# Performance work log

Measured on AMD Instinct MI355X. Metric: run time of the kernel, lower is better.

The kernel has to match this reference:

```python
import jax, jax.numpy as jnp
import numpy as np

# Production-scale config
N_NODES = 2048      # nodes in input graph
N_UND_EDGES = 4096  # undirected edges (avg degree ~4)
LABELS = 16         # node label categories
FILTERS = 16        # number of learned filter graphs
FNODES = 8          # nodes per filter graph ('nodes' init arg)
HOPS = 3            # egonet radius
MAX_EGO = 128       # egonet padding (covers typical 3-hop size at deg~4)
WL_LEVELS = 4       # initial labels + 3 WL refinements (n_iter=3)


def _mix(h):
    # 32-bit integer hash (lowbias32); equal colors -> equal hash, distinct w.h.p.
    h = h ^ (h >> jnp.uint32(16))
    h = h * jnp.uint32(0x7FEB352D)
    h = h ^ (h >> jnp.uint32(15))
    h = h * jnp.uint32(0x846CA68B)
    h = h ^ (h >> jnp.uint32(16))
    return h


def _wl_step(adj_u32, h):
    # multiset-hash WL relabel: new color = hash(old color, sum of hashed neighbor colors)
    msg = jnp.einsum('guv,gv->gu', adj_u32, _mix(h))  # uint32 wraparound sum
    return _mix(h * jnp.uint32(0x9E3779B1) + msg)


def _max_cc_mask(B):
    # largest connected component of a small binary graph via min-label propagation
    M = B.shape[0]
    lbl = jnp.arange(M)
    Bb = B > 0
    for _ in range(M):
        nb = jnp.min(jnp.where(Bb, lbl[None, :], M), axis=1)
        lbl = jnp.minimum(lbl, nb)
    cnt = (lbl[:, None] == lbl[None, :]).sum(1)
    return lbl == lbl[jnp.argmax(cnt)]


def setup_inputs() -> dict:
    key = jax.random.key(0)
    k1, k2, k3, k4, k5 = jax.random.split(key, 5)
    x = jax.random.normal(k1, (N_NODES, LABELS), dtype=jnp.float32)
    src = jax.random.randint(k2, (N_UND_EDGES,), 0, N_NODES)
    dst = jax.random.randint(k3, (N_UND_EDGES,), 0, N_NODES)
    edge_index = jnp.stack([jnp.concatenate([src, dst]),
                            jnp.concatenate([dst, src])]).astype(jnp.int32)
    batch = jnp.zeros((N_NODES,), dtype=jnp.int32)
    # filter adjacency exactly as in GKernel.__init__: symmetric binarized, zero diag
    Ar = jax.random.uniform(k4, (FILTERS, FNODES, FNODES))
    A = ((Ar + jnp.swapaxes(Ar, -2, -1)) > 1.0).astype(jnp.float32)
    A = A * (1.0 - jnp.eye(FNODES, dtype=jnp.float32))
    X = 10.0 * jax.random.normal(k5, (FILTERS, FNODES, LABELS), dtype=jnp.float32)
    return {"x": x, "edge_index": edge_index, "batch": batch, "A": A, "X": X}


def reference(x, edge_index, batch, A, X):
    N = x.shape[0]
    F, M = A.shape[0], A.shape[1]
    # dense symmetric adjacency of the input graph
    Adense = jnp.zeros((N, N), jnp.float32).at[edge_index[0], edge_index[1]].set(1.0)
    Adense = jnp.maximum(Adense, Adense.T)
    # 3-hop reachability (egonet membership), seed always included
    r = jnp.eye(N, dtype=jnp.float32)
    for _ in range(HOPS):
        r = ((r + r @ Adense) > 0).astype(jnp.float32)
    reach = r > 0
    ar = jnp.arange(N)
    # pick up to MAX_EGO member nodes per egonet (seed forced first)
    scores = reach.astype(jnp.int32) * (2 * N) - ar[None, :]
    scores = scores + jnp.where(ar[None, :] == ar[:, None], 8 * N, 0)
    _, idx = jax.lax.top_k(scores, MAX_EGO)                 # [N, K]
    emask = jnp.take_along_axis(reach, idx, axis=1).astype(jnp.float32)  # [N, K]
    adj_ego = Adense[idx[:, :, None], idx[:, None, :]] * emask[:, :, None] * emask[:, None, :]
    lab_e = jnp.argmax(x, -1)[idx]                          # [N, K] initial WL labels
    # filter graphs: keep only largest connected component (max_comp)
    fmask = jax.vmap(_max_cc_mask)(A).astype(jnp.float32)   # [F, M]
    Bf = A * fmask[:, :, None] * fmask[:, None, :]
    lab_f = jnp.argmax(X, -1)                               # [F, M]
    # WL color refinement + vertex-histogram kernel accumulation
    adj_e_u = adj_ego.astype(jnp.uint32)
    adj_f_u = Bf.astype(jnp.uint32)
    h_e = _mix(lab_e.astype(jnp.uint32) + jnp.uint32(1))
    h_f = _mix(lab_f.astype(jnp.uint32) + jnp.uint32(1))
    cross = jnp.zeros((N, F), jnp.float32)
    self_e = jnp.zeros((N,), jnp.float32)
    self_f = jnp.zeros((F,), jnp.float32)
    for t in range(WL_LEVELS):
        if t > 0:
            h_e = _wl_step(adj_e_u, h_e)
            h_f = _wl_step(adj_f_u, h_f)
        hf_flat = h_f.reshape(-1)                           # [F*M]
        eq = (h_e[:, :, None] == hf_flat[None, None, :]).astype(jnp.float32)  # [N,K,F*M]
        s = (eq * emask[:, :, None]).sum(1).reshape(N, F, M)
        cross = cross + (s * fmask[None]).sum(-1)
        eqee = (h_e[:, :, None] == h_e[:, None, :]).astype(jnp.float32)       # [N,K,K]
        self_e = self_e + (eqee * emask[:, :, None] * emask[:, None, :]).sum((1, 2))
        eqff = (h_f[:, :, None] == h_f[:, None, :]).astype(jnp.float32)       # [F,M,M]
        self_f = self_f + (eqff * fmask[:, :, None] * fmask[:, None, :]).sum((1, 2))
    sim = cross / jnp.sqrt(self_e[:, None] * self_f[None, :])  # normalized WL kernel
    return jnp.nan_to_num(sim)                              # [N, FILTERS]
```

## Files before the change

kernel.cpp:

```cpp
#include <hip/hip_runtime.h>
#include <hip/hip_bf16.h>
#include <stdint.h>

#define N_NODES 2048
#define WORDS   32
#define LABELS  16
#define FILTERS 16
#define FNODES  8
#define MAX_EGO 128
#define WL_LEVELS 4
#define IDCAP   256

typedef unsigned long long u64;

__device__ __forceinline__ unsigned mixu(unsigned h) {
    h ^= h >> 16; h *= 0x7FEB352Du;
    h ^= h >> 15; h *= 0x846CA68Bu;
    h ^= h >> 16;
    return h;
}

__global__ void __launch_bounds__(64)
build_adj_kernel(const int* __restrict__ ei, int E2, u64* __restrict__ Adense,
                 const float* __restrict__ Af, const float* __restrict__ Xf,
                 unsigned* __restrict__ hfg, unsigned* __restrict__ fmbg,
                 float* __restrict__ selfg) {
    const int lane = threadIdx.x;
    if ((int)blockIdx.x < (int)gridDim.x - 1) {
        int e = blockIdx.x * 64 + lane;
        if (e < E2) {
            int s = ei[e], d = ei[E2 + e];
            atomicOr(&Adense[(size_t)s * WORDS + (d >> 6)], 1ull << (d & 63));
            atomicOr(&Adense[(size_t)d * WORDS + (s >> 6)], 1ull << (s & 63));
        }
        return;
    }
    if (lane >= FILTERS) return;
    int f = lane;
    const float* Aff = Af + (size_t)f * FNODES * FNODES;
    unsigned row[FNODES];
    for (int m = 0; m < FNODES; ++m) {
        unsigned r = 0;
        for (int j = 0; j < FNODES; ++j)
            if (Aff[m * FNODES + j] > 0.f) r |= 1u << j;
        row[m] = r;
    }
    const float* Xff = Xf + (size_t)f * FNODES * LABELS;
    unsigned lab[FNODES];
    for (int m = 0; m < FNODES; ++m) {
        const float* xr = Xff + m * LABELS;
        float best = xr[0]; int bi = 0;
        for (int c = 1; c < LABELS; ++c) { float v = xr[c]; if (v > best) { best = v; bi = c; } }
        lab[m] = (unsigned)(bi + 1);
    }
    int lbl[FNODES];
    for (int m = 0; m < FNODES; ++m) lbl[m] = m;
    for (int it = 0; it < FNODES; ++it) {
        int nb2[FNODES];
        for (int m = 0; m < FNODES; ++m) {
            int mn = FNODES;
            for (int j = 0; j < FNODES; ++j)
                if ((row[m] >> j) & 1) mn = min(mn, lbl[j]);
            nb2[m] = mn;
        }
        for (int m = 0; m < FNODES; ++m) lbl[m] = min(lbl[m], nb2[m]);
    }
    int cnt[FNODES];
    for (int m = 0; m < FNODES; ++m) {
        int c = 0;
        for (int j = 0; j < FNODES; ++j) c += (lbl[j] == lbl[m]);
        cnt[m] = c;
    }
    int best = 0;
    for (int m = 1; m < FNODES; ++m) if (cnt[m] > cnt[best]) best = m;
    unsigned fm = 0;
    for (int m = 0; m < FNODES; ++m) if (lbl[m] == lbl[best]) fm |= 1u << m;
    fmbg[f] = fm;
    unsigned brow[FNODES];
    for (int m = 0; m < FNODES; ++m) brow[m] = ((fm >> m) & 1) ? (row[m] & fm) : 0u;
    unsigned hh[FNODES];
    for (int m = 0; m < FNODES; ++m) hh[m] = mixu(lab[m]);
    float sf = 0.f;
    for (int t = 0; t < WL_LEVELS; ++t) {
        if (t > 0) {
            unsigned mx[FNODES], nh[FNODES];
            for (int m = 0; m < FNODES; ++m) mx[m] = mixu(hh[m]);
            for (int m = 0; m < FNODES; ++m) {
                unsigned msg = 0;
                for (int j = 0; j < FNODES; ++j)
                    if ((brow[m] >> j) & 1) msg += mx[j];
                nh[m] = mixu(hh[m] * 0x9E3779B1u + msg);
            }
            for (int m = 0; m < FNODES; ++m) hh[m] = nh[m];
        }
        for (int m = 0; m < FNODES; ++m)
            hfg[t * FILTERS * FNODES + f * FNODES + m] = hh[m];
        int c = 0;
        for (int m = 0; m < FNODES; ++m) if ((fm >> m) & 1)
            for (int j = 0; j < FNODES; ++j) if ((fm >> j) & 1) c += (hh[m] == hh[j]);
        sf += (float)c;
    }
    selfg[f] = sf;
}

__global__ void __launch_bounds__(64)
ego_kernel(const float* __restrict__ x,
           const u64* __restrict__ Adense,
           const unsigned* __restrict__ hfg, const unsigned* __restrict__ fmbg,
           const float* __restrict__ selfg, float* __restrict__ out) {
    const int i    = blockIdx.x;
    const int lane = threadIdx.x;
    const int w    = lane & 31;
    const int hwp  = lane >> 5;

    __shared__ u64 arow[WORDS];
    __shared__ u64 r2s[WORDS];
    __shared__ u64 mmask[WORDS];
    __shared__ unsigned pfx[WORDS];
    __shared__ unsigned idlist[IDCAP];
    __shared__ unsigned members[MAX_EGO];
    __shared__ __align__(16) unsigned h[MAX_EGO];
    __shared__ unsigned mixed[MAX_EGO];
    __shared__ __align__(16) unsigned adjs[MAX_EGO][4];
    __shared__ unsigned hf_s[WL_LEVELS * FILTERS * FNODES];
    __shared__ unsigned fmb[FILTERS];
    __shared__ float    selff_s[FILTERS];
    __shared__ unsigned cross_sh[FILTERS];
    __shared__ unsigned selfe_sh;

    for (int t = lane; t < WL_LEVELS * FILTERS * FNODES; t += 64) hf_s[t] = hfg[t];
    if (lane < FILTERS) { fmb[lane] = fmbg[lane]; selff_s[lane] = selfg[lane]; }
    #pragma unroll
    for (int t = lane; t < MAX_EGO * 4; t += 64) ((unsigned*)adjs)[t] = 0;
    if (lane < WORDS) arow[lane] = Adense[(size_t)i * WORDS + lane];
    __syncthreads();

    int n1;
    {
        u64 v = arow[w];
        int pc = __popcll(v);
        int incl = pc;
        for (int d = 1; d < 32; d <<= 1) {
            int t2 = __shfl_up(incl, d, 32);
            if (w >= d) incl += t2;
        }
        int ex = incl - pc;
        u64 vv = v; int r = 0;
        while (vv) {
            int b = __ffsll(vv) - 1; vv &= vv - 1;
            if (ex + r < IDCAP) idlist[ex + r] = (unsigned)((w << 6) + b);
            ++r;
        }
        n1 = min(__shfl(incl, 31, 32), IDCAP);
    }
    __syncthreads();

    u64 racc = arow[w];
    if ((i >> 6) == w) racc |= 1ull << (i & 63);
    for (int t = hwp; t < n1; t += 8) {
        int t1 = t + 2, t2 = t + 4, t3 = t + 6;
        u64 v0 = Adense[(size_t)idlist[t] * WORDS + w];
        u64 v1 = (t1 < n1) ? Adense[(size_t)idlist[t1] * WORDS + w] : 0ull;
        u64 v2 = (t2 < n1) ? Adense[(size_t)idlist[t2] * WORDS + w] : 0ull;
        u64 v3 = (t3 < n1) ? Adense[(size_t)idlist[t3] * WORDS + w] : 0ull;
        racc |= v0 | v1 | v2 | v3;
    }
    racc |= __shfl_xor(racc, 32, 64);
    r2s[w] = racc;
    __syncthreads();

    int n2;
    {
        u64 v = r2s[w];
        int pc = __popcll(v);
        int incl = pc;
        for (int d = 1; d < 32; d <<= 1) {
            int t2 = __shfl_up(incl, d, 32);
            if (w >= d) incl += t2;
        }
        int ex = incl - pc;
        u64 vv = v; int r = 0;
        while (vv) {
            int b = __ffsll(vv) - 1; vv &= vv - 1;
            if (ex + r < IDCAP) idlist[ex + r] = (unsigned)((w << 6) + b);
            ++r;
        }
        n2 = min(__shfl(incl, 31, 32), IDCAP);
    }
    __syncthreads();

    u64 acc3 = racc;
    for (int t = hwp; t < n2; t += 8) {
        int t1 = t + 2, t2 = t + 4, t3 = t + 6;
        u64 v0 = Adense[(size_t)idlist[t] * WORDS + w];
        u64 v1 = (t1 < n2) ? Adense[(size_t)idlist[t1] * WORDS + w] : 0ull;
        u64 v2 = (t2 < n2) ? Adense[(size_t)idlist[t2] * WORDS + w] : 0ull;
        u64 v3 = (t3 < n2) ? Adense[(size_t)idlist[t3] * WORDS + w] : 0ull;
        acc3 |= v0 | v1 | v2 | v3;
    }
    acc3 |= __shfl_xor(acc3, 32, 64);

    int S;
    {
        u64 v = acc3;
        int seedw = i >> 6;
        u64 seedbit = 1ull << (i & 63);
        if (w == seedw) v &= ~seedbit;
        int pc = __popcll(v);
        int incl = pc;
        for (int d = 1; d < 32; d <<= 1) {
            int t2 = __shfl_up(incl, d, 32);
            if (w >= d) incl += t2;
        }
        int excl = incl - pc;
        const int keep = MAX_EGO - 1;
        if (excl >= keep) {
            v = 0;
        } else {
            int allow = keep - excl;
            while (pc > allow) {
                v &= ~(1ull << (63 - __clzll(v)));
                --pc;
            }
        }
        if (w == seedw) v |= seedbit;
        mmask[w] = v;
        int pc2 = __popcll(v);
        int incl2 = pc2;
        for (int d = 1; d < 32; d <<= 1) {
            int t2 = __shfl_up(incl2, d, 32);
            if (w >= d) incl2 += t2;
        }
        int ex2 = incl2 - pc2;
        pfx[w] = (unsigned)ex2;
        u64 vv = v;
        int r = 0;
        while (vv) {
            int b = __ffsll(vv) - 1;
            vv &= vv - 1;
            members[ex2 + r] = (unsigned)((w << 6) + b);
            ++r;
        }
        S = __shfl(incl2, 31, 32);
    }
    __syncthreads();
    const int s0 = lane, s1 = lane + 64;
    const bool p0 = (s0 < S), p1 = (s1 < S);

    {
        unsigned hl0 = 0, hl1 = 0;
        if (p0) {
            const float4* xr = (const float4*)(x + (size_t)members[s0] * LABELS);
            float4 a0 = xr[0], a1 = xr[1], a2 = xr[2], a3 = xr[3];
            float vv[16] = {a0.x,a0.y,a0.z,a0.w,a1.x,a1.y,a1.z,a1.w,
                            a2.x,a2.y,a2.z,a2.w,a3.x,a3.y,a3.z,a3.w};
            float best = vv[0]; int bi = 0;
            #pragma unroll
            for (int c = 1; c < 16; ++c) { if (vv[c] > best) { best = vv[c]; bi = c; } }
            hl0 = mixu((unsigned)(bi + 1));
        }
        if (p1) {
            const float4* xr = (const float4*)(x + (size_t)members[s1] * LABELS);
            float4 a0 = xr[0], a1 = xr[1], a2 = xr[2], a3 = xr[3];
            float vv[16] = {a0.x,a0.y,a0.z,a0.w,a1.x,a1.y,a1.z,a1.w,
                            a2.x,a2.y,a2.z,a2.w,a3.x,a3.y,a3.z,a3.w};
            float best = vv[0]; int bi = 0;
            #pragma unroll
            for (int c = 1; c < 16; ++c) { if (vv[c] > best) { best = vv[c]; bi = c; } }
            hl1 = mixu((unsigned)(bi + 1));
        }
        if (p0) h[s0] = hl0;
        if (p1) h[s1] = hl1;
    }

    {
        const u64 mw = mmask[w];
        const unsigned base = pfx[w];
        for (int t = hwp; t < S; t += 8) {
            int t1 = t + 2, t2 = t + 4, t3 = t + 6;
            u64 v0 = Adense[(size_t)members[t] * WORDS + w] & mw;
            u64 v1 = (t1 < S) ? (Adense[(size_t)members[t1] * WORDS + w] & mw) : 0ull;
            u64 v2 = (t2 < S) ? (Adense[(size_t)members[t2] * WORDS + w] & mw) : 0ull;
            u64 v3 = (t3 < S) ? (Adense[(size_t)members[t3] * WORDS + w] & mw) : 0ull;
            while (v0) {
                int b = __ffsll(v0) - 1; v0 &= v0 - 1;
                int slot = (int)base + __popcll(mw & ((1ull << b) - 1));
                atomicOr(&adjs[t][slot >> 5], 1u << (slot & 31));
            }
            while (v1) {
                int b = __ffsll(v1) - 1; v1 &= v1 - 1;
                int slot = (int)base + __popcll(mw & ((1ull << b) - 1));
                atomicOr(&adjs[t1][slot >> 5], 1u << (slot & 31));
            }
            while (v2) {
                int b = __ffsll(v2) - 1; v2 &= v2 - 1;
                int slot = (int)base + __popcll(mw & ((1ull << b) - 1));
                atomicOr(&adjs[t2][slot >> 5], 1u << (slot & 31));
            }
            while (v3) {
                int b = __ffsll(v3) - 1; v3 &= v3 - 1;
                int slot = (int)base + __popcll(mw & ((1ull << b) - 1));
                atomicOr(&adjs[t3][slot >> 5], 1u << (slot & 31));
            }
        }
    }
    __syncthreads();

    unsigned crossReg[FILTERS];
    #pragma unroll
    for (int f = 0; f < FILTERS; ++f) crossReg[f] = 0;
    unsigned selfeReg = 0;

    for (int t = 0; t < WL_LEVELS; ++t) {
        if (t > 0) {
            if (p0) mixed[s0] = mixu(h[s0]);
            if (p1) mixed[s1] = mixu(h[s1]);
            __syncthreads();
            unsigned hn0 = 0, hn1 = 0;
            if (p0) {
                unsigned msg = 0;
                uint4 aw = *(const uint4*)adjs[s0];
                unsigned bw[4] = {aw.x, aw.y, aw.z, aw.w};
                #pragma unroll
                for (int ww = 0; ww < 4; ++ww) {
                    unsigned bits = bw[ww];
                    while (bits) { int l = __ffs(bits) - 1; bits &= bits - 1; msg += mixed[(ww << 5) + l]; }
                }
                hn0 = mixu(h[s0] * 0x9E3779B1u + msg);
            }
            if (p1) {
                unsigned msg = 0;
                uint4 aw = *(const uint4*)adjs[s1];
                unsigned bw[4] = {aw.x, aw.y, aw.z, aw.w};
                #pragma unroll
                for (int ww = 0; ww < 4; ++ww) {
                    unsigned bits = bw[ww];
                    while (bits) { int l = __ffs(bits) - 1; bits &= bits - 1; msg += mixed[(ww << 5) + l]; }
                }
                hn1 = mixu(h[s1] * 0x9E3779B1u + msg);
            }
            __syncthreads();
            if (p0) h[s0] = hn0;
            if (p1) h[s1] = hn1;
            __syncthreads();
        }

        const unsigned hv0 = p0 ? h[s0] : 0u;
        const unsigned hv1 = p1 ? h[s1] : 0u;
        const unsigned* hrow = &hf_s[t * FILTERS * FNODES];
        if (p0) {
            #pragma unroll
            for (int f = 0; f < FILTERS; ++f) {
                unsigned fm = fmb[f], c = 0;
                #pragma unroll
                for (int m = 0; m < FNODES; ++m)
                    c += (unsigned)((hv0 == hrow[f * FNODES + m]) & ((fm >> m) & 1u));
                crossReg[f] += c;
            }
        }
        if (p1) {
            #pragma unroll
            for (int f = 0; f < FILTERS; ++f) {
                unsigned fm = fmb[f], c = 0;
                #pragma unroll
                for (int m = 0; m < FNODES; ++m)
                    c += (unsigned)((hv1 == hrow[f * FNODES + m]) & ((fm >> m) & 1u));
                crossReg[f] += c;
            }
        }
        {
            unsigned ce = 0;
            const int quads = S >> 2;
            const uint4* h4 = (const uint4*)h;
            for (int qq = 0; qq < quads; ++qq) {
                uint4 hh = h4[qq];
                if (p0) ce += (unsigned)(hh.x == hv0) + (unsigned)(hh.y == hv0)
                            + (unsigned)(hh.z == hv0) + (unsigned)(hh.w == hv0);
                if (p1) ce += (unsigned)(hh.x == hv1) + (unsigned)(hh.y == hv1)
                            + (unsigned)(hh.z == hv1) + (unsigned)(hh.w == hv1);
            }
            for (int l = quads << 2; l < S; ++l) {
                unsigned hl = h[l];
                if (p0) ce += (unsigned)(hl == hv0);
                if (p1) ce += (unsigned)(hl == hv1);
            }
            selfeReg += ce;
        }
        __syncthreads();
    }

    #pragma unroll
    for (int f = 0; f < FILTERS; ++f) {
        unsigned v = crossReg[f];
        for (int o = 32; o > 0; o >>= 1) v += __shfl_down(v, o, 64);
        crossReg[f] = v;
    }
    {
        unsigned v = selfeReg;
        for (int o = 32; o > 0; o >>= 1) v += __shfl_down(v, o, 64);
        selfeReg = v;
    }
    if (lane == 0) {
        #pragma unroll
        for (int f = 0; f < FILTERS; ++f) cross_sh[f] = crossReg[f];
        selfe_sh = selfeReg;
    }
    __syncthreads();
    if (lane < FILTERS) {
        float se = (float)selfe_sh;
        float sf = selff_s[lane];
        float denom = sqrtf(se * sf);
        float v = (denom > 0.f) ? ((float)cross_sh[lane] / denom) : 0.f;
        out[(size_t)i * FILTERS + lane] = v;
    }
}

extern "C" void kernel_launch(void* const* d_in, const int* in_sizes, int n_in,
                              void* d_out, int out_size, void* d_ws, size_t ws_size,
                              hipStream_t stream) {
    const float* x  = (const float*)d_in[0];
    const int*   ei = (const int*)d_in[1];
    const float* A  = (const float*)d_in[3];
    const float* X  = (const float*)d_in[4];
    float* out = (float*)d_out;
    int E2 = in_sizes[1] / 2;

    char* ws = (char*)d_ws;
    const size_t ADJ_BYTES = (size_t)N_NODES * WORDS * sizeof(u64);
    u64* Adense = (u64*)(ws);
    unsigned* hfg    = (unsigned*)(ws + ADJ_BYTES);
    unsigned* fmbg   = (unsigned*)(ws + ADJ_BYTES + 4096);
    float*    selfg  = (float*)  (ws + ADJ_BYTES + 4096 + 256);

    hipMemsetAsync(Adense, 0, ADJ_BYTES, stream);
    int nbE = (E2 + 63) / 64;
    build_adj_kernel<<<nbE + 1, 64, 0, stream>>>(ei, E2, Adense, A, X, hfg, fmbg, selfg);
    ego_kernel<<<N_NODES, 64, 0, stream>>>(x, Adense, hfg, fmbg, selfg, out);
}
```

Measured before the change: 131.4 us.

## Scatter WL messages via LDS atomics and deepen adjacency gather unroll

The WL message step changes from a pull gather over precomputed mixed hashes to a push scatter: each node atomically adds its own mixed hash into its neighbours' LDS accumulators. Node hashes and adjacency rows are now kept in registers across levels, which removes the repeated LDS reads of h and adjs. The BFS and adjacency-build loops now issue 8 global loads per iteration instead of 4, for more memory-level parallelism. The LDS atomic adds may contend on high-degree nodes, and the wider unroll raises register pressure.

```diff
diff --git a/kernel.cpp b/kernel.cpp
--- a/kernel.cpp
+++ b/kernel.cpp
@@ -120,7 +120,7 @@
     __shared__ unsigned idlist[IDCAP];
     __shared__ unsigned members[MAX_EGO];
     __shared__ __align__(16) unsigned h[MAX_EGO];
-    __shared__ unsigned mixed[MAX_EGO];
+    __shared__ unsigned msgacc[MAX_EGO];
     __shared__ __align__(16) unsigned adjs[MAX_EGO][4];
     __shared__ unsigned hf_s[WL_LEVELS * FILTERS * FNODES];
     __shared__ unsigned fmb[FILTERS];
@@ -157,13 +157,14 @@
 
     u64 racc = arow[w];
     if ((i >> 6) == w) racc |= 1ull << (i & 63);
-    for (int t = hwp; t < n1; t += 8) {
-        int t1 = t + 2, t2 = t + 4, t3 = t + 6;
-        u64 v0 = Adense[(size_t)idlist[t] * WORDS + w];
-        u64 v1 = (t1 < n1) ? Adense[(size_t)idlist[t1] * WORDS + w] : 0ull;
-        u64 v2 = (t2 < n1) ? Adense[(size_t)idlist[t2] * WORDS + w] : 0ull;
-        u64 v3 = (t3 < n1) ? Adense[(size_t)idlist[t3] * WORDS + w] : 0ull;
-        racc |= v0 | v1 | v2 | v3;
+    for (int t = hwp; t < n1; t += 16) {
+        u64 vb[8];
+        #pragma unroll
+        for (int k = 0; k < 8; ++k) {
+            int tk = t + 2 * k;
+            vb[k] = (tk < n1) ? Adense[(size_t)idlist[tk] * WORDS + w] : 0ull;
+        }
+        racc |= vb[0] | vb[1] | vb[2] | vb[3] | vb[4] | vb[5] | vb[6] | vb[7];
     }
     racc |= __shfl_xor(racc, 32, 64);
     r2s[w] = racc;
@@ -190,13 +191,14 @@
     __syncthreads();
 
     u64 acc3 = racc;
-    for (int t = hwp; t < n2; t += 8) {
-        int t1 = t + 2, t2 = t + 4, t3 = t + 6;
-        u64 v0 = Adense[(size_t)idlist[t] * WORDS + w];
-        u64 v1 = (t1 < n2) ? Adense[(size_t)idlist[t1] * WORDS + w] : 0ull;
-        u64 v2 = (t2 < n2) ? Adense[(size_t)idlist[t2] * WORDS + w] : 0ull;
-        u64 v3 = (t3 < n2) ? Adense[(size_t)idlist[t3] * WORDS + w] : 0ull;
-        acc3 |= v0 | v1 | v2 | v3;
+    for (int t = hwp; t < n2; t += 16) {
+        u64 vb[8];
+        #pragma unroll
+        for (int k = 0; k < 8; ++k) {
+            int tk = t + 2 * k;
+            vb[k] = (tk < n2) ? Adense[(size_t)idlist[tk] * WORDS + w] : 0ull;
+        }
+        acc3 |= vb[0] | vb[1] | vb[2] | vb[3] | vb[4] | vb[5] | vb[6] | vb[7];
     }
     acc3 |= __shfl_xor(acc3, 32, 64);
 
@@ -247,8 +249,8 @@
     const int s0 = lane, s1 = lane + 64;
     const bool p0 = (s0 < S), p1 = (s1 < S);
 
-    {
-        unsigned hl0 = 0, hl1 = 0;
+    unsigned hv0 = 0, hv1 = 0;
+    {
         if (p0) {
             const float4* xr = (const float4*)(x + (size_t)members[s0] * LABELS);
             float4 a0 = xr[0], a1 = xr[1], a2 = xr[2], a3 = xr[3];
@@ -257,7 +259,8 @@
             float best = vv[0]; int bi = 0;
             #pragma unroll
             for (int c = 1; c < 16; ++c) { if (vv[c] > best) { best = vv[c]; bi = c; } }
-            hl0 = mixu((unsigned)(bi + 1));
+            hv0 = mixu((unsigned)(bi + 1));
+            h[s0] = hv0;
         }
         if (p1) {
             const float4* xr = (const float4*)(x + (size_t)members[s1] * LABELS);
@@ -267,44 +270,37 @@
             float best = vv[0]; int bi = 0;
             #pragma unroll
             for (int c = 1; c < 16; ++c) { if (vv[c] > best) { best = vv[c]; bi = c; } }
-            hl1 = mixu((unsigned)(bi + 1));
-        }
-        if (p0) h[s0] = hl0;
-        if (p1) h[s1] = hl1;
+            hv1 = mixu((unsigned)(bi + 1));
+            h[s1] = hv1;
+        }
     }
 
     {
         const u64 mw = mmask[w];
         const unsigned base = pfx[w];
-        for (int t = hwp; t < S; t += 8) {
-            int t1 = t + 2, t2 = t + 4, t3 = t + 6;
-            u64 v0 = Adense[(size_t)members[t] * WORDS + w] & mw;
-            u64 v1 = (t1 < S) ? (Adense[(size_t)members[t1] * WORDS + w] & mw) : 0ull;
-            u64 v2 = (t2 < S) ? (Adense[(size_t)members[t2] * WORDS + w] & mw) : 0ull;
-            u64 v3 = (t3 < S) ? (Adense[(size_t)members[t3] * WORDS + w] & mw) : 0ull;
-            while (v0) {
-                int b = __ffsll(v0) - 1; v0 &= v0 - 1;
-                int slot = (int)base + __popcll(mw & ((1ull << b) - 1));
-                atomicOr(&adjs[t][slot >> 5], 1u << (slot & 31));
-            }
-            while (v1) {
-                int b = __ffsll(v1) - 1; v1 &= v1 - 1;
-                int slot = (int)base + __popcll(mw & ((1ull << b) - 1));
-                atomicOr(&adjs[t1][slot >> 5], 1u << (slot & 31));
-            }
-            while (v2) {
-                int b = __ffsll(v2) - 1; v2 &= v2 - 1;
-                int slot = (int)base + __popcll(mw & ((1ull << b) - 1));
-                atomicOr(&adjs[t2][slot >> 5], 1u << (slot & 31));
-            }
-            while (v3) {
-                int b = __ffsll(v3) - 1; v3 &= v3 - 1;
-                int slot = (int)base + __popcll(mw & ((1ull << b) - 1));
-                atomicOr(&adjs[t3][slot >> 5], 1u << (slot & 31));
-            }
-        }
-    }
-    __syncthreads();
+        for (int t = hwp; t < S; t += 16) {
+            u64 vb[8];
+            int ti[8];
+            #pragma unroll
+            for (int k = 0; k < 8; ++k) {
+                ti[k] = t + 2 * k;
+                vb[k] = (ti[k] < S) ? (Adense[(size_t)members[ti[k]] * WORDS + w] & mw) : 0ull;
+            }
+            #pragma unroll
+            for (int k = 0; k < 8; ++k) {
+                u64 v = vb[k];
+                while (v) {
+                    int b = __ffsll(v) - 1; v &= v - 1;
+                    int slot = (int)base + __popcll(mw & ((1ull << b) - 1));
+                    atomicOr(&adjs[ti[k]][slot >> 5], 1u << (slot & 31));
+                }
+            }
+        }
+    }
+    __syncthreads();
+
+    uint4 aw0 = *(const uint4*)adjs[s0];
+    uint4 aw1 = *(const uint4*)adjs[s1];
 
     unsigned crossReg[FILTERS];
     #pragma unroll
@@ -313,40 +309,34 @@
 
     for (int t = 0; t < WL_LEVELS; ++t) {
         if (t > 0) {
-            if (p0) mixed[s0] = mixu(h[s0]);
-            if (p1) mixed[s1] = mixu(h[s1]);
+            msgacc[lane] = 0u; msgacc[lane + 64] = 0u;
             __syncthreads();
-            unsigned hn0 = 0, hn1 = 0;
             if (p0) {
-                unsigned msg = 0;
-                uint4 aw = *(const uint4*)adjs[s0];
-                unsigned bw[4] = {aw.x, aw.y, aw.z, aw.w};
+                unsigned mixv = mixu(hv0);
+                unsigned bw[4] = {aw0.x, aw0.y, aw0.z, aw0.w};
                 #pragma unroll
                 for (int ww = 0; ww < 4; ++ww) {
                     unsigned bits = bw[ww];
-                    while (bits) { int l = __ffs(bits) - 1; bits &= bits - 1; msg += mixed[(ww << 5) + l]; }
+                    while (bits) { int l = __ffs(bits) - 1; bits &= bits - 1;
+                                   atomicAdd(&msgacc[(ww << 5) + l], mixv); }
                 }
-                hn0 = mixu(h[s0] * 0x9E3779B1u + msg);
             }
             if (p1) {
-                unsigned msg = 0;
-                uint4 aw = *(const uint4*)adjs[s1];
-                unsigned bw[4] = {aw.x, aw.y, aw.z, aw.w};
+                unsigned mixv = mixu(hv1);
+                unsigned bw[4] = {aw1.x, aw1.y, aw1.z, aw1.w};
                 #pragma unroll
                 for (int ww = 0; ww < 4; ++ww) {
                     unsigned bits = bw[ww];
-                    while (bits) { int l = __ffs(bits) - 1; bits &= bits - 1; msg += mixed[(ww << 5) + l]; }
+                    while (bits) { int l = __ffs(bits) - 1; bits &= bits - 1;
+                                   atomicAdd(&msgacc[(ww << 5) + l], mixv); }
                 }
-                hn1 = mixu(h[s1] * 0x9E3779B1u + msg);
             }
             __syncthreads();
-            if (p0) h[s0] = hn0;
-            if (p1) h[s1] = hn1;
+            if (p0) { hv0 = mixu(hv0 * 0x9E3779B1u + msgacc[s0]); h[s0] = hv0; }
+            if (p1) { hv1 = mixu(hv1 * 0x9E3779B1u + msgacc[s1]); h[s1] = hv1; }
             __syncthreads();
         }
 
-        const unsigned hv0 = p0 ? h[s0] : 0u;
-        const unsigned hv1 = p1 ? h[s1] : 0u;
         const unsigned* hrow = &hf_s[t * FILTERS * FNODES];
         if (p0) {
             #pragma unroll
```

New measurement: 130.7 us. About the same (-0.6%).
